# Optimization experiments

Hardware: AMD Instinct MI355X
Metric: run time of the kernel (lower is better)

The kernel has to match this reference:

```python
import jax, jax.numpy as jnp
import numpy as np

B = 8            # scenes per batch
N_PER = 100_000  # voxels per scene
C_IN = 32
C_OUT = 64
GRID = 128       # voxel grid extent per axis
K = 8            # 2x2x2 kernel offsets
EPS = 1e-5


def _kernel_maps():
    """Build stride-2 sparse-conv kernel maps (MinkowskiEngine semantics).

    Each input voxel at coord c maps to output voxel floor(c/2) with kernel
    offset c - 2*floor(c/2) in {0,1}^3.
    """
    rng = np.random.default_rng(0)
    coords = rng.integers(0, GRID, size=(B * N_PER, 3)).astype(np.int64)
    batch = np.repeat(np.arange(B, dtype=np.int64), N_PER)
    out_c = coords // 2
    off = coords - 2 * out_c                      # {0,1}^3
    k_idx = off[:, 0] * 4 + off[:, 1] * 2 + off[:, 2]
    half = GRID // 2
    key = ((batch * half + out_c[:, 0]) * half + out_c[:, 1]) * half + out_c[:, 2]
    _, out_idx = np.unique(key, return_inverse=True)
    num_out = int(out_idx.max()) + 1
    return k_idx.astype(np.int32), out_idx.astype(np.int32), num_out


def setup_inputs() -> dict:
    k_idx_np, out_idx_np, num_out = _kernel_maps()
    key = jax.random.key(0)
    k1, k2, k3 = jax.random.split(key, 3)
    x = jax.random.normal(k1, (B * N_PER, C_IN), dtype=jnp.float32)
    W = jax.random.normal(k2, (K, C_IN, C_OUT), dtype=jnp.float32) * 0.05
    bias = jax.random.normal(k3, (C_OUT,), dtype=jnp.float32) * 0.01
    gamma = jnp.ones((C_OUT,), dtype=jnp.float32)
    beta = jnp.zeros((C_OUT,), dtype=jnp.float32)
    return {
        "x": x, "W": W, "bias": bias, "gamma": gamma, "beta": beta,
        "k_idx": jnp.asarray(k_idx_np), "out_idx": jnp.asarray(out_idx_np),
        "num_out": num_out,
    }


def reference(x, W, bias, gamma, beta, k_idx, out_idx, num_out):
    # Sparse conv (gather-GEMM-scatter). Each input voxel uses exactly one of
    # the 8 kernel weights (stride==kernel_size==2), so y[i] = x[i] @ W[k_idx[i]].
    y = jnp.zeros((x.shape[0], W.shape[2]), dtype=x.dtype)
    for j in range(K):  # small fixed loop over kernel offsets
        y = y + jnp.where((k_idx == j)[:, None], x @ W[j], 0.0)
    out = jax.ops.segment_sum(y, out_idx, num_segments=num_out) + bias
    # BatchNorm (training-mode batch stats over output voxels) + ReLU
    mean = out.mean(axis=0)
    var = out.var(axis=0)
    out = (out - mean) * jax.lax.rsqrt(var + EPS) * gamma + beta
    return jax.nn.relu(out)
```

## Files before the change

### kernel.cpp

```cpp
#include <hip/hip_runtime.h>

#define EPS_BN 1e-5f

typedef __attribute__((ext_vector_type(8))) short short8;
typedef __attribute__((ext_vector_type(4))) float floatx4;

__device__ __forceinline__ short f2bf(float f) {
    unsigned u = __float_as_uint(f);
    u += 0x7FFF + ((u >> 16) & 1);
    return (short)(u >> 16);
}
__device__ __forceinline__ float bf2f(short s) {
    return __uint_as_float(((unsigned)(unsigned short)s) << 16);
}


__global__ void scatter_pack(const int* __restrict__ out_idx,
                             const int* __restrict__ k_idx,
                             const float* __restrict__ W,
                             int* __restrict__ slot, int* __restrict__ next,
                             unsigned* __restrict__ cm_inv,
                             short* __restrict__ packed, int n)
{
    const int i = blockIdx.x * 256 + threadIdx.x;
    if (blockIdx.x < 8) {
        const int s = i;
        const int j = s >> 8, t = (s >> 6) & 3, l = s & 63;
        const int k0 = (l >> 4) * 8, c = (l & 15) + 16 * t;
        short8 v;
#pragma unroll
        for (int q = 0; q < 8; ++q)
            v[q] = f2bf(W[(j * 32 + k0 + q) * 64 + c]);
        ((short8*)packed)[s] = v;
    }
    if (i < n) {
        const int o = out_idx[i];
        const int k = k_idx[i];
        int old = atomicExch(&slot[(size_t)o * 8 + k], i);
        next[i] = old;
        if (old >= 0) atomicAnd(&cm_inv[o], ~(1u << k));
    }
}

template <bool YB16>
__global__ __launch_bounds__(512, 8) void gather_mfma(
    const float* __restrict__ x, const short* __restrict__ packedW,
    const int* __restrict__ slot, const int* __restrict__ next_arr,
    const unsigned* __restrict__ cm_inv,
    float* __restrict__ out, short* __restrict__ yb,
    float* __restrict__ partials, int num_out, int nb)
{
    __shared__ short sW[16384];
    __shared__ float s_stat[128];

    const int tid = threadIdx.x;
    const int wave = tid >> 6, lane = tid & 63;
    const int quad = lane >> 4, row = lane & 15;
    const int obase = blockIdx.x * 128 + wave * 16;
    const int o = obase + row;
    const bool valid_o = (o < num_out);

    int4 sl0 = make_int4(-1, -1, -1, -1), sl1 = sl0;
    unsigned cmraw = 0xFFFFFFFFu;
    if (valid_o) {
        const int4* sp = (const int4*)(slot + (size_t)o * 8);
        sl0 = sp[0]; sl1 = sp[1];
        cmraw = cm_inv[o];
    }

    if (tid < 128) s_stat[tid] = 0.f;
    for (int i = tid; i < 2048; i += 512)
        ((short8*)sW)[i] = ((const short8*)packedW)[i];
    __syncthreads();

    const unsigned cm = ~cmraw;

    floatx4 acc[4] = {{0,0,0,0},{0,0,0,0},{0,0,0,0},{0,0,0,0}};
    const short8* bw = (const short8*)sW;

#pragma unroll
    for (int j = 0; j < 8; ++j) {
        const int v = (j < 4) ? ((j == 0) ? sl0.x : (j == 1) ? sl0.y : (j == 2) ? sl0.z : sl0.w)
                              : ((j == 4) ? sl1.x : (j == 5) ? sl1.y : (j == 6) ? sl1.z : sl1.w);
        if (!__any(v >= 0)) continue;
        float4 xa = make_float4(0.f, 0.f, 0.f, 0.f), xb = xa;
        if (v >= 0) {
            const float4* xp = (const float4*)(x + (size_t)v * 32) + quad * 2;
            xa = xp[0]; xb = xp[1];
        }
        if (__builtin_expect(__any((cm >> j) & 1u), 0)) {
            int w = (v >= 0 && ((cm >> j) & 1u)) ? next_arr[v] : -1;
            while (__any(w >= 0)) {
                if (w >= 0) {
                    const float4* xp2 = (const float4*)(x + (size_t)w * 32) + quad * 2;
                    float4 ya = xp2[0], yb4 = xp2[1];
                    xa.x += ya.x; xa.y += ya.y; xa.z += ya.z; xa.w += ya.w;
                    xb.x += yb4.x; xb.y += yb4.y; xb.z += yb4.z; xb.w += yb4.w;
                    w = next_arr[w];
                }
            }
        }
        short8 afrag;
        afrag[0] = f2bf(xa.x); afrag[1] = f2bf(xa.y);
        afrag[2] = f2bf(xa.z); afrag[3] = f2bf(xa.w);
        afrag[4] = f2bf(xb.x); afrag[5] = f2bf(xb.y);
        afrag[6] = f2bf(xb.z); afrag[7] = f2bf(xb.w);

        const int jb = j * 256;
#pragma unroll
        for (int t = 0; t < 4; ++t) {
            const short8 bfrag = bw[jb + t * 64 + lane];
            acc[t] = __builtin_amdgcn_mfma_f32_16x16x32_bf16(afrag, bfrag, acc[t], 0, 0, 0);
        }
    }

    if constexpr (YB16) {
        __syncthreads();
        short* ylds = sW;
#pragma unroll
        for (int t = 0; t < 4; ++t) {
            const int c = (lane & 15) + 16 * t;
            float sum = 0.f, sq = 0.f;
#pragma unroll
            for (int r = 0; r < 4; ++r) {
                const int rl = quad * 4 + r;
                const float val = acc[t][r];
                ylds[wave * 1024 + rl * 64 + c] = f2bf(val);
                if (obase + rl < num_out) { sum += val; sq += val * val; }
            }
            sum += __shfl_xor(sum, 16, 64); sum += __shfl_xor(sum, 32, 64);
            sq  += __shfl_xor(sq, 16, 64);  sq  += __shfl_xor(sq, 32, 64);
            if (quad == 0) {
                atomicAdd(&s_stat[c], sum);
                atomicAdd(&s_stat[64 + c], sq);
            }
        }
        __syncthreads();
        const size_t rbase = (size_t)blockIdx.x * 128;
#pragma unroll
        for (int k = 0; k < 2; ++k) {
            const int i = tid + k * 512;
            if (rbase + (i >> 3) < (size_t)num_out)
                ((short8*)yb)[rbase * 8 + i] = ((const short8*)ylds)[i];
        }
    } else {
#pragma unroll
        for (int t = 0; t < 4; ++t) {
            const int c = (lane & 15) + 16 * t;
            float sum = 0.f, sq = 0.f;
#pragma unroll
            for (int r = 0; r < 4; ++r) {
                const int oc = obase + quad * 4 + r;
                const float val = acc[t][r];
                if (oc < num_out) {
                    out[(size_t)oc * 64 + c] = val;
                    sum += val; sq += val * val;
                }
            }
            sum += __shfl_xor(sum, 16, 64); sum += __shfl_xor(sum, 32, 64);
            sq  += __shfl_xor(sq, 16, 64);  sq  += __shfl_xor(sq, 32, 64);
            if (quad == 0) {
                atomicAdd(&s_stat[c], sum);
                atomicAdd(&s_stat[64 + c], sq);
            }
        }
        __syncthreads();
    }
    if (tid < 128) partials[(size_t)tid * nb + blockIdx.x] = s_stat[tid];
}

__global__ __launch_bounds__(256) void reduce_finalize(
    const float* __restrict__ partials, const float* __restrict__ gamma,
    const float* __restrict__ beta, float* __restrict__ ws_ab,
    int nb, float inv_n)
{
    __shared__ float r1[256], r2[256];
    const int c = blockIdx.x, t = threadIdx.x;
    float s1 = 0.f, s2 = 0.f;
    for (int i = t; i < nb; i += 256) {
        s1 += partials[(size_t)c * nb + i];
        s2 += partials[(size_t)(c + 64) * nb + i];
    }
    r1[t] = s1; r2[t] = s2;
    __syncthreads();
    for (int d = 128; d > 0; d >>= 1) {
        if (t < d) { r1[t] += r1[t + d]; r2[t] += r2[t + d]; }
        __syncthreads();
    }
    if (t == 0) {
        const float mean = r1[0] * inv_n;
        const float var = r2[0] * inv_n - mean * mean;
        const float a = gamma[c] * rsqrtf(var + EPS_BN);
        ws_ab[c] = a;
        ws_ab[64 + c] = beta[c] - mean * a;
    }
}

__global__ __launch_bounds__(256) void apply_bf16(
    const short* __restrict__ yb, float* __restrict__ out,
    const float* __restrict__ ws_ab, int ngroups)
{
    const int tid = blockIdx.x * 256 + threadIdx.x;
    const int stride = gridDim.x * 256;
    const int g = tid & 7;
    float a[8], b[8];
#pragma unroll
    for (int q = 0; q < 8; ++q) {
        a[q] = ws_ab[g * 8 + q];
        b[q] = ws_ab[64 + g * 8 + q];
    }
    const short8* y8 = (const short8*)yb;
    floatx4* o4 = (floatx4*)out;
    for (int i = tid; i < ngroups; i += stride) {
        const short8 v = y8[i];
        floatx4 o0, o1;
        o0.x = fmaxf(fmaf(bf2f(v[0]), a[0], b[0]), 0.f);
        o0.y = fmaxf(fmaf(bf2f(v[1]), a[1], b[1]), 0.f);
        o0.z = fmaxf(fmaf(bf2f(v[2]), a[2], b[2]), 0.f);
        o0.w = fmaxf(fmaf(bf2f(v[3]), a[3], b[3]), 0.f);
        o1.x = fmaxf(fmaf(bf2f(v[4]), a[4], b[4]), 0.f);
        o1.y = fmaxf(fmaf(bf2f(v[5]), a[5], b[5]), 0.f);
        o1.z = fmaxf(fmaf(bf2f(v[6]), a[6], b[6]), 0.f);
        o1.w = fmaxf(fmaf(bf2f(v[7]), a[7], b[7]), 0.f);
        __builtin_nontemporal_store(o0, o4 + (size_t)i * 2);
        __builtin_nontemporal_store(o1, o4 + (size_t)i * 2 + 1);
    }
}

__global__ __launch_bounds__(256) void apply_f32(
    float* __restrict__ out, const float* __restrict__ ws_ab, int n4)
{
    const int tid = blockIdx.x * 256 + threadIdx.x;
    const int stride = gridDim.x * 256;
    const int cg = tid & 15;
    const floatx4 a = ((const floatx4*)ws_ab)[cg];
    const floatx4 b = ((const floatx4*)(ws_ab + 64))[cg];
    floatx4* o4 = (floatx4*)out;
    for (int i = tid; i < n4; i += stride) {
        floatx4 v = o4[i];
        v.x = fmaxf(fmaf(v.x, a.x, b.x), 0.f);
        v.y = fmaxf(fmaf(v.y, a.y, b.y), 0.f);
        v.z = fmaxf(fmaf(v.z, a.z, b.z), 0.f);
        v.w = fmaxf(fmaf(v.w, a.w, b.w), 0.f);
        __builtin_nontemporal_store(v, o4 + i);
    }
}

extern "C" void kernel_launch(void* const* d_in, const int* in_sizes, int n_in,
                              void* d_out, int out_size, void* d_ws, size_t ws_size,
                              hipStream_t stream)
{
    const float* x     = (const float*)d_in[0];
    const float* W     = (const float*)d_in[1];
    const float* gamma = (const float*)d_in[3];
    const float* beta  = (const float*)d_in[4];
    const int* k_idx   = (const int*)d_in[5];
    const int* out_idx = (const int*)d_in[6];

    const int n_vox   = in_sizes[5];
    const int num_out = out_size / 64;
    const int nb      = (num_out + 127) / 128;
    float* out = (float*)d_out;

    char* p = (char*)d_ws;
    float* ws_ab    = (float*)(p + 512);
    short* packedW  = (short*)(p + 1024);
    float* partials = (float*)(p + 1024 + 32768);
    size_t off      = 1024 + 32768 + (size_t)128 * nb * 4;
    int*   slot     = (int*)(p + off);
    unsigned* cm_inv = (unsigned*)(slot + (size_t)num_out * 8);
    int*   next     = (int*)(cm_inv + num_out);
    size_t ybOff    = (off + (size_t)num_out * 36 + (size_t)n_vox * 4 + 15) & ~(size_t)15;
    short* yb       = (short*)(p + ybOff);
    const bool useBf16 = (ws_size >= ybOff + (size_t)num_out * 128);

    (void)hipMemsetAsync(slot, 0xFF, (size_t)num_out * 9 * sizeof(int), stream);

    const int nsb = (n_vox + 255) / 256;
    scatter_pack  <<<nsb, 256, 0, stream>>>(out_idx, k_idx, W, slot, next, cm_inv, packedW, n_vox);
    if (useBf16) {
        gather_mfma<true><<<nb, 512, 0, stream>>>(x, packedW, slot, next, cm_inv, out, yb, partials, num_out, nb);
        reduce_finalize<<<64, 256, 0, stream>>>(partials, gamma, beta, ws_ab, nb, 1.0f / (float)num_out);
        apply_bf16 <<<4096, 256, 0, stream>>>(yb, out, ws_ab, num_out * 8);
    } else {
        gather_mfma<false><<<nb, 512, 0, stream>>>(x, packedW, slot, next, cm_inv, out, yb, partials, num_out, nb);
        reduce_finalize<<<64, 256, 0, stream>>>(partials, gamma, beta, ws_ab, nb, 1.0f / (float)num_out);
        apply_f32  <<<4096, 256, 0, stream>>>(out, ws_ab, out_size / 4);
    }
}
```

Before: 413.2 us.

## Use persistent grid-stride blocks in gather kernel with register-accumulated BN stats

Caps the gather-MFMA grid at 1024 blocks that loop over 128-row output tiles, accumulating per-channel sum and sum-of-squares in registers and reducing once per block. This shrinks the partials array and the final reduction, and cuts per-block launch and shared-atomic overhead. In exchange it reloads weights into LDS every tile, adds an extra barrier per tile, and may reduce resident waves available to hide gather latency.

```diff
diff --git a/kernel.cpp b/kernel.cpp
--- a/kernel.cpp
+++ b/kernel.cpp
@@ -48,7 +48,7 @@
     const int* __restrict__ slot, const int* __restrict__ next_arr,
     const unsigned* __restrict__ cm_inv,
     float* __restrict__ out, short* __restrict__ yb,
-    float* __restrict__ partials, int num_out, int nb)
+    float* __restrict__ partials, int num_out, int ntiles)
 {
     __shared__ short sW[16384];
     __shared__ float s_stat[128];
@@ -56,117 +56,126 @@
     const int tid = threadIdx.x;
     const int wave = tid >> 6, lane = tid & 63;
     const int quad = lane >> 4, row = lane & 15;
-    const int obase = blockIdx.x * 128 + wave * 16;
-    const int o = obase + row;
-    const bool valid_o = (o < num_out);
-
-    int4 sl0 = make_int4(-1, -1, -1, -1), sl1 = sl0;
-    unsigned cmraw = 0xFFFFFFFFu;
-    if (valid_o) {
-        const int4* sp = (const int4*)(slot + (size_t)o * 8);
-        sl0 = sp[0]; sl1 = sp[1];
-        cmraw = cm_inv[o];
-    }
+    const short8* bw = (const short8*)sW;
 
     if (tid < 128) s_stat[tid] = 0.f;
-    for (int i = tid; i < 2048; i += 512)
-        ((short8*)sW)[i] = ((const short8*)packedW)[i];
+
+    float statS[4] = {0.f, 0.f, 0.f, 0.f};
+    float statQ[4] = {0.f, 0.f, 0.f, 0.f};
+
+    for (int tile = blockIdx.x; tile < ntiles; tile += gridDim.x) {
+        const int obase = tile * 128 + wave * 16;
+        const int o = obase + row;
+        const bool valid_o = (o < num_out);
+
+        int4 sl0 = make_int4(-1, -1, -1, -1), sl1 = sl0;
+        unsigned cmraw = 0xFFFFFFFFu;
+        if (valid_o) {
+            const int4* sp = (const int4*)(slot + (size_t)o * 8);
+            sl0 = sp[0]; sl1 = sp[1];
+            cmraw = cm_inv[o];
+        }
+
+        for (int i = tid; i < 2048; i += 512)
+            ((short8*)sW)[i] = ((const short8*)packedW)[i];
+        __syncthreads();
+
+        const unsigned cm = ~cmraw;
+
+        floatx4 acc[4] = {{0,0,0,0},{0,0,0,0},{0,0,0,0},{0,0,0,0}};
+
+#pragma unroll
+        for (int j = 0; j < 8; ++j) {
+            const int v = (j < 4) ? ((j == 0) ? sl0.x : (j == 1) ? sl0.y : (j == 2) ? sl0.z : sl0.w)
+                                  : ((j == 4) ? sl1.x : (j == 5) ? sl1.y : (j == 6) ? sl1.z : sl1.w);
+            if (!__any(v >= 0)) continue;
+            float4 xa = make_float4(0.f, 0.f, 0.f, 0.f), xb = xa;
+            if (v >= 0) {
+                const float4* xp = (const float4*)(x + (size_t)v * 32) + quad * 2;
+                xa = xp[0]; xb = xp[1];
+            }
+            if (__builtin_expect(__any((cm >> j) & 1u), 0)) {
+                int w = (v >= 0 && ((cm >> j) & 1u)) ? next_arr[v] : -1;
+                while (__any(w >= 0)) {
+                    if (w >= 0) {
+                        const float4* xp2 = (const float4*)(x + (size_t)w * 32) + quad * 2;
+                        float4 ya = xp2[0], yb4 = xp2[1];
+                        xa.x += ya.x; xa.y += ya.y; xa.z += ya.z; xa.w += ya.w;
+                        xb.x += yb4.x; xb.y += yb4.y; xb.z += yb4.z; xb.w += yb4.w;
+                        w = next_arr[w];
+                    }
+                }
+            }
+            short8 afrag;
+            afrag[0] = f2bf(xa.x); afrag[1] = f2bf(xa.y);
+            afrag[2] = f2bf(xa.z); afrag[3] = f2bf(xa.w);
+            afrag[4] = f2bf(xb.x); afrag[5] = f2bf(xb.y);
+            afrag[6] = f2bf(xb.z); afrag[7] = f2bf(xb.w);
+
+            const int jb = j * 256;
+#pragma unroll
+            for (int t = 0; t < 4; ++t) {
+                const short8 bfrag = bw[jb + t * 64 + lane];
+                acc[t] = __builtin_amdgcn_mfma_f32_16x16x32_bf16(afrag, bfrag, acc[t], 0, 0, 0);
+            }
+        }
+
+        if constexpr (YB16) {
+            __syncthreads();
+            short* ylds = sW;
+#pragma unroll
+            for (int t = 0; t < 4; ++t) {
+#pragma unroll
+                for (int r = 0; r < 4; ++r) {
+                    const int rl = quad * 4 + r;
+                    const int c = (lane & 15) + 16 * t;
+                    const float val = acc[t][r];
+                    ylds[wave * 1024 + rl * 64 + c] = f2bf(val);
+                    if (obase + rl < num_out) {
+                        statS[t] += val; statQ[t] += val * val;
+                    }
+                }
+            }
+            __syncthreads();
+            const size_t rbase = (size_t)tile * 128;
+#pragma unroll
+            for (int k = 0; k < 2; ++k) {
+                const int i = tid + k * 512;
+                if (rbase + (i >> 3) < (size_t)num_out)
+                    ((short8*)yb)[rbase * 8 + i] = ((const short8*)ylds)[i];
+            }
+            __syncthreads();
+        } else {
+#pragma unroll
+            for (int t = 0; t < 4; ++t) {
+                const int c = (lane & 15) + 16 * t;
+#pragma unroll
+                for (int r = 0; r < 4; ++r) {
+                    const int oc = obase + quad * 4 + r;
+                    const float val = acc[t][r];
+                    if (oc < num_out) {
+                        out[(size_t)oc * 64 + c] = val;
+                        statS[t] += val; statQ[t] += val * val;
+                    }
+                }
+            }
+            __syncthreads();
+        }
+    }
+
+#pragma unroll
+    for (int t = 0; t < 4; ++t) {
+        float sum = statS[t], sq = statQ[t];
+        sum += __shfl_xor(sum, 16, 64); sum += __shfl_xor(sum, 32, 64);
+        sq  += __shfl_xor(sq, 16, 64);  sq  += __shfl_xor(sq, 32, 64);
+        if (quad == 0) {
+            const int c = (lane & 15) + 16 * t;
+            atomicAdd(&s_stat[c], sum);
+            atomicAdd(&s_stat[64 + c], sq);
+        }
+    }
     __syncthreads();
-
-    const unsigned cm = ~cmraw;
-
-    floatx4 acc[4] = {{0,0,0,0},{0,0,0,0},{0,0,0,0},{0,0,0,0}};
-    const short8* bw = (const short8*)sW;
-
-#pragma unroll
-    for (int j = 0; j < 8; ++j) {
-        const int v = (j < 4) ? ((j == 0) ? sl0.x : (j == 1) ? sl0.y : (j == 2) ? sl0.z : sl0.w)
-                              : ((j == 4) ? sl1.x : (j == 5) ? sl1.y : (j == 6) ? sl1.z : sl1.w);
-        if (!__any(v >= 0)) continue;
-        float4 xa = make_float4(0.f, 0.f, 0.f, 0.f), xb = xa;
-        if (v >= 0) {
-            const float4* xp = (const float4*)(x + (size_t)v * 32) + quad * 2;
-            xa = xp[0]; xb = xp[1];
-        }
-        if (__builtin_expect(__any((cm >> j) & 1u), 0)) {
-            int w = (v >= 0 && ((cm >> j) & 1u)) ? next_arr[v] : -1;
-            while (__any(w >= 0)) {
-                if (w >= 0) {
-                    const float4* xp2 = (const float4*)(x + (size_t)w * 32) + quad * 2;
-                    float4 ya = xp2[0], yb4 = xp2[1];
-                    xa.x += ya.x; xa.y += ya.y; xa.z += ya.z; xa.w += ya.w;
-                    xb.x += yb4.x; xb.y += yb4.y; xb.z += yb4.z; xb.w += yb4.w;
-                    w = next_arr[w];
-                }
-            }
-        }
-        short8 afrag;
-        afrag[0] = f2bf(xa.x); afrag[1] = f2bf(xa.y);
-        afrag[2] = f2bf(xa.z); afrag[3] = f2bf(xa.w);
-        afrag[4] = f2bf(xb.x); afrag[5] = f2bf(xb.y);
-        afrag[6] = f2bf(xb.z); afrag[7] = f2bf(xb.w);
-
-        const int jb = j * 256;
-#pragma unroll
-        for (int t = 0; t < 4; ++t) {
-            const short8 bfrag = bw[jb + t * 64 + lane];
-            acc[t] = __builtin_amdgcn_mfma_f32_16x16x32_bf16(afrag, bfrag, acc[t], 0, 0, 0);
-        }
-    }
-
-    if constexpr (YB16) {
-        __syncthreads();
-        short* ylds = sW;
-#pragma unroll
-        for (int t = 0; t < 4; ++t) {
-            const int c = (lane & 15) + 16 * t;
-            float sum = 0.f, sq = 0.f;
-#pragma unroll
-            for (int r = 0; r < 4; ++r) {
-                const int rl = quad * 4 + r;
-                const float val = acc[t][r];
-                ylds[wave * 1024 + rl * 64 + c] = f2bf(val);
-                if (obase + rl < num_out) { sum += val; sq += val * val; }
-            }
-            sum += __shfl_xor(sum, 16, 64); sum += __shfl_xor(sum, 32, 64);
-            sq  += __shfl_xor(sq, 16, 64);  sq  += __shfl_xor(sq, 32, 64);
-            if (quad == 0) {
-                atomicAdd(&s_stat[c], sum);
-                atomicAdd(&s_stat[64 + c], sq);
-            }
-        }
-        __syncthreads();
-        const size_t rbase = (size_t)blockIdx.x * 128;
-#pragma unroll
-        for (int k = 0; k < 2; ++k) {
-            const int i = tid + k * 512;
-            if (rbase + (i >> 3) < (size_t)num_out)
-                ((short8*)yb)[rbase * 8 + i] = ((const short8*)ylds)[i];
-        }
-    } else {
-#pragma unroll
-        for (int t = 0; t < 4; ++t) {
-            const int c = (lane & 15) + 16 * t;
-            float sum = 0.f, sq = 0.f;
-#pragma unroll
-            for (int r = 0; r < 4; ++r) {
-                const int oc = obase + quad * 4 + r;
-                const float val = acc[t][r];
-                if (oc < num_out) {
-                    out[(size_t)oc * 64 + c] = val;
-                    sum += val; sq += val * val;
-                }
-            }
-            sum += __shfl_xor(sum, 16, 64); sum += __shfl_xor(sum, 32, 64);
-            sq  += __shfl_xor(sq, 16, 64);  sq  += __shfl_xor(sq, 32, 64);
-            if (quad == 0) {
-                atomicAdd(&s_stat[c], sum);
-                atomicAdd(&s_stat[64 + c], sq);
-            }
-        }
-        __syncthreads();
-    }
-    if (tid < 128) partials[(size_t)tid * nb + blockIdx.x] = s_stat[tid];
+    if (tid < 128) partials[(size_t)tid * gridDim.x + blockIdx.x] = s_stat[tid];
 }
 
 __global__ __launch_bounds__(256) void reduce_finalize(
@@ -259,14 +268,15 @@
 
     const int n_vox   = in_sizes[5];
     const int num_out = out_size / 64;
-    const int nb      = (num_out + 127) / 128;
+    const int ntiles  = (num_out + 127) / 128;
+    const int nbg     = (ntiles < 1024) ? ntiles : 1024;
     float* out = (float*)d_out;
 
     char* p = (char*)d_ws;
     float* ws_ab    = (float*)(p + 512);
     short* packedW  = (short*)(p + 1024);
     float* partials = (float*)(p + 1024 + 32768);
-    size_t off      = 1024 + 32768 + (size_t)128 * nb * 4;
+    size_t off      = 1024 + 32768 + (size_t)128 * nbg * 4;
     int*   slot     = (int*)(p + off);
     unsigned* cm_inv = (unsigned*)(slot + (size_t)num_out * 8);
     int*   next     = (int*)(cm_inv + num_out);
@@ -279,12 +289,12 @@
     const int nsb = (n_vox + 255) / 256;
     scatter_pack  <<<nsb, 256, 0, stream>>>(out_idx, k_idx, W, slot, next, cm_inv, packedW, n_vox);
     if (useBf16) {
-        gather_mfma<true><<<nb, 512, 0, stream>>>(x, packedW, slot, next, cm_inv, out, yb, partials, num_out, nb);
-        reduce_finalize<<<64, 256, 0, stream>>>(partials, gamma, beta, ws_ab, nb, 1.0f / (float)num_out);
+        gather_mfma<true><<<nbg, 512, 0, stream>>>(x, packedW, slot, next, cm_inv, out, yb, partials, num_out, ntiles);
+        reduce_finalize<<<64, 256, 0, stream>>>(partials, gamma, beta, ws_ab, nbg, 1.0f / (float)num_out);
         apply_bf16 <<<4096, 256, 0, stream>>>(yb, out, ws_ab, num_out * 8);
     } else {
-        gather_mfma<false><<<nb, 512, 0, stream>>>(x, packedW, slot, next, cm_inv, out, yb, partials, num_out, nb);
-        reduce_finalize<<<64, 256, 0, stream>>>(partials, gamma, beta, ws_ab, nb, 1.0f / (float)num_out);
+        gather_mfma<false><<<nbg, 512, 0, stream>>>(x, packedW, slot, next, cm_inv, out, yb, partials, num_out, ntiles);
+        reduce_finalize<<<64, 256, 0, stream>>>(partials, gamma, beta, ws_ab, nbg, 1.0f / (float)num_out);
         apply_f32  <<<4096, 256, 0, stream>>>(out, ws_ab, out_size / 4);
     }
 }
```

Result: no change. 419.7 us (+1.6%).
